# Kernel tuning notes

Hardware: AMD Instinct MI355X
Metric: run time of the kernel (lower is better)

Reference implementation:

```python
import jax, jax.numpy as jnp
import numpy as np

N_VERTICES = 2000
N_SENSORY = 784
N_EDGES = 500_000
BATCH = 32
T_STEPS = 5
LR_VALUES = 0.1


def setup_inputs() -> dict:
    key = jax.random.key(0)
    k1, k2, k3 = jax.random.split(key, 3)
    values = jax.random.normal(k1, (BATCH, N_VERTICES), dtype=jnp.float32)
    # weight_init 'normal 0.0' -> std = max(0.01, 0) = 0.01 in the torch module
    weights = jax.random.normal(k2, (N_EDGES,), dtype=jnp.float32) * 0.01
    edge_index = jax.random.randint(k3, (2, N_EDGES), 0, N_VERTICES, dtype=jnp.int32)
    # sensory nodes (first 784) are clamped; only internal nodes update
    update_mask = jnp.arange(N_VERTICES) >= N_SENSORY  # bool [N]
    return {
        "values": values,
        "weights": weights,
        "edge_index": edge_index,
        "update_mask": update_mask,
        "T": T_STEPS,
    }


def reference(values, weights, edge_index, update_mask, T):
    """Iterative predictive-coding message passing.

    Each step:
      pred_i  = sum_{e: dst(e)=i} w_e * f(values[src(e)])   (gather-mul-scatter)
      err     = values - pred
      back_j  = sum_{e: src(e)=j} w_e * err[dst(e)]          (reverse scatter)
      dv      = err - f'(values) * back                      (dE/dx)
      values  = values - lr * dv   (sensory nodes clamped)
    """
    src, dst = edge_index[0], edge_index[1]
    n = values.shape[1]
    mask = update_mask[None, :]

    def step(v, _):
        fx = jnp.tanh(v)                                   # [B, N]
        msg = weights[None, :] * fx[:, src]                # [B, E]
        pred = jax.ops.segment_sum(msg.T, dst, num_segments=n).T  # [B, N]
        err = v - pred                                     # [B, N]
        w_err = weights[None, :] * err[:, dst]             # [B, E]
        back = jax.ops.segment_sum(w_err.T, src, num_segments=n).T  # [B, N]
        fprime = 1.0 - fx * fx                             # tanh'
        dv = err - fprime * back
        v_new = jnp.where(mask, v - LR_VALUES * dv, v)
        return v_new, None

    v_final, _ = jax.lax.scan(step, values, None, length=T)
    return v_final
```

## Files before the change

### kernel.cpp

```cpp
#include <hip/hip_runtime.h>
#include <hip/hip_bf16.h>


#define N_V     2000
#define N_SENS  784
#define N_INT   (N_V - N_SENS)
#define N_E     500000
#define T_STEPS 5
#define LR_VAL  0.1f
#define NVB     (N_V * 32)
#define NVH     (N_V * 16)
#define KP      2016
#define NCH     63
#define NT1     125
#define NT2     76
#define FRAG_N  (2 * NCH * 64 * 8)
#define NBLK    250
#define EPB     2000
#define NBLK_P  NT1
#define BAR_STRIDE 32
#define BAR_N   ((NBLK_P + 1) * BAR_STRIDE)

typedef float  f32x4 __attribute__((ext_vector_type(4)));
typedef short  s16x8 __attribute__((ext_vector_type(8)));
typedef unsigned long long u64;

__device__ __forceinline__ float bits_to_f32(unsigned u) {
    union { unsigned u; float f; } c; c.u = u; return c.f;
}
__device__ __forceinline__ unsigned f32_to_bits(float f) {
    union { float f; unsigned u; } c; c.f = f; return c.u;
}
__device__ __forceinline__ unsigned short f32_to_bf16(float f) {
    unsigned u = f32_to_bits(f);
    return (unsigned short)((u + 0x7FFFu + ((u >> 16) & 1u)) >> 16);
}
__device__ __forceinline__ float bf16_to_f32(unsigned short s) {
    return bits_to_f32((unsigned)s << 16);
}

__device__ __forceinline__ u64 ald64(const void* p) {
    return __hip_atomic_load((const u64*)p, __ATOMIC_RELAXED,
                             __HIP_MEMORY_SCOPE_AGENT);
}
__device__ __forceinline__ void ast64(void* p, u64 v) {
    __hip_atomic_store((u64*)p, v, __ATOMIC_RELAXED, __HIP_MEMORY_SCOPE_AGENT);
}
__device__ __forceinline__ unsigned short ald16(const unsigned short* p) {
    return __hip_atomic_load(p, __ATOMIC_RELAXED, __HIP_MEMORY_SCOPE_AGENT);
}
__device__ __forceinline__ void ast16(unsigned short* p, unsigned short v) {
    __hip_atomic_store(p, v, __ATOMIC_RELAXED, __HIP_MEMORY_SCOPE_AGENT);
}
__device__ __forceinline__ int cohld(const int* p) {
    int v;
    asm volatile("global_load_dword %0, %1, off sc0 sc1\n\ts_waitcnt vmcnt(0)"
                 : "=v"(v) : "v"(p) : "memory");
    return v;
}
__device__ __forceinline__ void cohst(int* p, int v) {
    asm volatile("global_store_dword %0, %1, off sc0 sc1"
                 :: "v"(p), "v"(v) : "memory");
}

__device__ __forceinline__ int aposKB(int k, int b) {
    int c = k >> 5, q = (k >> 3) & 3, j = k & 7;
    int h = b >> 4, m = b & 15;
    return (((h * NCH + c) * 64) + q * 16 + m) * 8 + j;
}


__global__ __launch_bounds__(256) void k_cnt(const int* __restrict__ dst,
                                             int* __restrict__ cnt_g,
                                             unsigned short* __restrict__ fxA,
                                             unsigned short* __restrict__ errA,
                                             const float* __restrict__ vin,
                                             float* __restrict__ v,
                                             float* __restrict__ out,
                                             unsigned short* __restrict__ WAdT,
                                             int* __restrict__ bar) {
    __shared__ int cnt[NT1];
    int b = blockIdx.x;
    int t = b * 256 + threadIdx.x;
    {
        if (t < 16 * 32) {
            int k = 2000 + (t >> 5), bb = t & 31;
            fxA[aposKB(k, bb)] = 0;
            errA[aposKB(k, bb)] = 0;
        }
        if (t < N_INT * 2) {
            uint4 z = {0u, 0u, 0u, 0u};
            *(uint4*)(WAdT + (size_t)(t >> 1) * KP + 2000 + (t & 1) * 8) = z;
        }
        if (t < BAR_N) bar[t] = 0;
    }
    if (t < NVB) {
        float x = vin[t];
        int bb = t / N_V;
        int i = t - bb * N_V;
        v[(i << 5) + bb] = x;
        fxA[aposKB(i, bb)] = f32_to_bf16(tanhf(x));
        if (i < N_SENS) out[t] = x;
    }
    for (int i = threadIdx.x; i < NT1; i += 256) cnt[i] = 0;
    __syncthreads();
    int base = b * EPB;
    for (int e = base + threadIdx.x; e < base + EPB; e += 256)
        atomicAdd(&cnt[dst[e] >> 4], 1);
    __syncthreads();
    for (int tt = threadIdx.x; tt < NT1; tt += 256)
        cnt_g[tt * 256 + b] = cnt[tt];
}

__global__ __launch_bounds__(256) void k_scan_a(const int* __restrict__ cnt_g,
                                                int* __restrict__ base_g,
                                                int* __restrict__ totals) {
    __shared__ int sh[256];
    int t = blockIdx.x, tid = threadIdx.x;
    int v = (tid < NBLK) ? cnt_g[t * 256 + tid] : 0;
    sh[tid] = v;
    __syncthreads();
    for (int off = 1; off < 256; off <<= 1) {
        int x = (tid >= off) ? sh[tid - off] : 0;
        __syncthreads();
        sh[tid] += x;
        __syncthreads();
    }
    if (tid < NBLK) base_g[t * 256 + tid] = sh[tid] - v;
    if (tid == 255) totals[t] = sh[255];
}

__global__ __launch_bounds__(256) void k_place(
        const int* __restrict__ src, const int* __restrict__ dst,
        const float* __restrict__ w, const int* __restrict__ base_g,
        const int* __restrict__ totals, unsigned* __restrict__ pk_g) {
    __shared__ int cur[NT1];
    __shared__ int ts[NT1];
    int b = blockIdx.x;
    if (threadIdx.x == 0) {
        int a = 0;
        for (int t = 0; t < NT1; ++t) { ts[t] = a; a += totals[t]; }
    }
    __syncthreads();
    for (int t = threadIdx.x; t < NT1; t += 256)
        cur[t] = ts[t] + base_g[t * 256 + b];
    __syncthreads();
    int base = b * EPB;
    for (int e = base + threadIdx.x; e < base + EPB; e += 256) {
        int d = dst[e];
        unsigned pk = ((unsigned)f32_to_bf16(w[e]) << 16)
                    | ((unsigned)(d & 15) << 11) | (unsigned)src[e];
        int p = atomicAdd(&cur[d >> 4], 1);
        pk_g[p] = pk;
    }
}

__global__ __launch_bounds__(256) void k_build(
        const unsigned* __restrict__ pk_g, const int* __restrict__ totals,
        uint4* __restrict__ WAbf4, unsigned short* __restrict__ WAdT) {
    __shared__ float acc[16][KP];
    __shared__ int ts[NT1 + 1];
    int tile = blockIdx.x;
    for (int i = threadIdx.x; i < 16 * KP / 4; i += 256)
        ((float4*)&acc[0][0])[i] = make_float4(0.f, 0.f, 0.f, 0.f);
    if (threadIdx.x == 0) {
        int a = 0;
        for (int t = 0; t < NT1; ++t) { ts[t] = a; a += totals[t]; }
        ts[NT1] = a;
    }
    __syncthreads();
    int beg = ts[tile], end = ts[tile + 1];
    for (int e = beg + threadIdx.x; e < end; e += 256) {
        unsigned pk = pk_g[e];
        int row = (int)((pk >> 11) & 15u);
        atomicAdd(&acc[row][pk & 0x7FFu], bf16_to_f32((unsigned short)(pk >> 16)));
    }
    __syncthreads();
    for (int i = threadIdx.x; i < 16 * 252; i += 256) {
        int m = i / 252, g = i - m * 252;
        int c = g >> 2, q = g & 3;
        int col = g * 8;
        unsigned short r[8];
        #pragma unroll
        for (int j = 0; j < 8; ++j) r[j] = f32_to_bf16(acc[m][col + j]);
        WAbf4[((tile * NCH + c) * 64) + q * 16 + m] = *(const uint4*)r;
    }
    for (int i = threadIdx.x; i < N_INT; i += 256) {
        int j = N_SENS + i;
        unsigned short r[16];
        #pragma unroll
        for (int m = 0; m < 16; ++m) r[m] = f32_to_bf16(acc[m][j]);
        uint4* p = (uint4*)(WAdT + (size_t)i * KP + tile * 16);
        p[0] = *(const uint4*)r;
        p[1] = *(const uint4*)(r + 8);
    }
}

__device__ __forceinline__ void gbar(int* arr, int epoch, int bx, int tid) {
    asm volatile("s_waitcnt vmcnt(0) lgkmcnt(0)" ::: "memory");
    __syncthreads();
    if (bx == 0) {
        if (tid == 0) cohst(&arr[0], epoch);
        if (tid < NBLK_P) {
            while (cohld(&arr[tid * BAR_STRIDE]) < epoch)
                __builtin_amdgcn_s_sleep(2);
        }
        __syncthreads();
        if (tid == 0) cohst(&arr[NBLK_P * BAR_STRIDE], epoch);
    } else {
        if (tid == 0) {
            cohst(&arr[bx * BAR_STRIDE], epoch);
            while (cohld(&arr[NBLK_P * BAR_STRIDE]) < epoch)
                __builtin_amdgcn_s_sleep(2);
        }
        __syncthreads();
    }
}

__global__ __launch_bounds__(512, 1) void k_loop(
        const uint4* __restrict__ WAbf4, const unsigned short* __restrict__ WAdT,
        unsigned short* fxA, unsigned short* errA,
        float* v_cur, float* __restrict__ out, int* arr) {
    __shared__ uint4 WldsA[NCH * 64];
    __shared__ uint4 WldsB[NCH * 64];
    __shared__ float red[2600];
    const int bx = blockIdx.x, tid = threadIdx.x;
    {
        const uint4* Wg = WAbf4 + (size_t)bx * (NCH * 64);
        for (int i = tid; i < NCH * 64; i += 512) WldsA[i] = Wg[i];
        if (bx < NT2) {
            for (int i = tid; i < NCH * 64; i += 512) {
                int c = i >> 6, ll = i & 63;
                int row = bx * 16 + (ll & 15);
                int k0 = c * 32 + (ll >> 4) * 8;
                WldsB[i] = *(const uint4*)(WAdT + (size_t)row * KP + k0);
            }
        }
    }
    const int w = tid >> 6, l = tid & 63;
    const int h = w >> 2, w4 = w & 3;
    const int cbeg = w4 * 16;
    float* my = &red[h * 1300 + w4 * 325 + l * 5];
    int epoch = 0;
    __syncthreads();

    for (int t = 0; t < T_STEPS; ++t) {
        {
            const u64* ap = (const u64*)fxA
                          + ((size_t)h * (NCH * 64) + cbeg * 64 + l) * 2;
            u64 f0[16], f1[16];
            #pragma unroll
            for (int cc = 0; cc < 16; ++cc)
                if (cbeg + cc < NCH) {
                    f0[cc] = ald64(ap + cc * 128);
                    f1[cc] = ald64(ap + cc * 128 + 1);
                }
            __builtin_amdgcn_sched_barrier(0);
            f32x4 acc = {0.f, 0.f, 0.f, 0.f};
            #pragma unroll
            for (int cc = 0; cc < 16; ++cc)
                if (cbeg + cc < NCH) {
                    u64 d[2] = {f0[cc], f1[cc]};
                    uint4 bfrag = WldsA[(cbeg + cc) * 64 + l];
                    acc = __builtin_amdgcn_mfma_f32_16x16x32_bf16(
                              *(s16x8*)d, *(s16x8*)&bfrag, acc, 0, 0, 0);
                }
            #pragma unroll
            for (int r = 0; r < 4; ++r) my[r] = acc[r];
            __syncthreads();
            if (w4 == 0) {
                float s[4];
                #pragma unroll
                for (int r = 0; r < 4; ++r)
                    s[r] = red[h * 1300 + l * 5 + r] + red[h * 1300 + 325 + l * 5 + r]
                         + red[h * 1300 + 650 + l * 5 + r] + red[h * 1300 + 975 + l * 5 + r];
                int i = bx * 16 + (l & 15);
                int q = l >> 4;
                int c2 = i >> 5, q2 = (i >> 3) & 3, j2 = i & 7;
                const float* vp = v_cur + (i << 5) + h * 16 + q * 4;
                union { u64 u[2]; float f[4]; } vu;
                vu.u[0] = ald64(vp);
                vu.u[1] = ald64(vp + 2);
                int base = ((h * NCH + c2) * 64 + q2 * 16) * 8 + j2;
                #pragma unroll
                for (int r = 0; r < 4; ++r)
                    ast16(&errA[base + (q * 4 + r) * 8],
                          f32_to_bf16(vu.f[r] - s[r]));
            }
        }
        ++epoch; gbar(arr, epoch, bx, tid);

        if (bx < NT2) {
            const u64* ap = (const u64*)errA
                          + ((size_t)h * (NCH * 64) + cbeg * 64 + l) * 2;
            u64 f0[16], f1[16];
            #pragma unroll
            for (int cc = 0; cc < 16; ++cc)
                if (cbeg + cc < NCH) {
                    f0[cc] = ald64(ap + cc * 128);
                    f1[cc] = ald64(ap + cc * 128 + 1);
                }
            __builtin_amdgcn_sched_barrier(0);
            f32x4 acc = {0.f, 0.f, 0.f, 0.f};
            #pragma unroll
            for (int cc = 0; cc < 16; ++cc)
                if (cbeg + cc < NCH) {
                    u64 d[2] = {f0[cc], f1[cc]};
                    uint4 bfrag = WldsB[(cbeg + cc) * 64 + l];
                    acc = __builtin_amdgcn_mfma_f32_16x16x32_bf16(
                              *(s16x8*)d, *(s16x8*)&bfrag, acc, 0, 0, 0);
                }
            #pragma unroll
            for (int r = 0; r < 4; ++r) my[r] = acc[r];
            __syncthreads();
            if (w4 == 0) {
                float s[4];
                #pragma unroll
                for (int r = 0; r < 4; ++r)
                    s[r] = red[h * 1300 + l * 5 + r] + red[h * 1300 + 325 + l * 5 + r]
                         + red[h * 1300 + 650 + l * 5 + r] + red[h * 1300 + 975 + l * 5 + r];
                int j = N_SENS + bx * 16 + (l & 15);
                int q = l >> 4;
                int c2 = j >> 5, q2 = (j >> 3) & 3, j2 = j & 7;
                float* vp = v_cur + (j << 5) + h * 16 + q * 4;
                union { u64 u[2]; float f[4]; } vu;
                vu.u[0] = ald64(vp);
                vu.u[1] = ald64(vp + 2);
                int base = ((h * NCH + c2) * 64 + q2 * 16) * 8 + j2;
                #pragma unroll
                for (int r = 0; r < 4; ++r) {
                    float e0 = bf16_to_f32(ald16(&errA[base + (q * 4 + r) * 8]));
                    float fxv = tanhf(vu.f[r]);
                    float vn = vu.f[r] - LR_VAL * (e0 - (1.f - fxv * fxv) * s[r]);
                    vu.f[r] = vn;
                    ast16(&fxA[base + (q * 4 + r) * 8], f32_to_bf16(tanhf(vn)));
                }
                ast64(vp, vu.u[0]);
                ast64(vp + 2, vu.u[1]);
                if (t == T_STEPS - 1) {
                    #pragma unroll
                    for (int r = 0; r < 4; ++r) {
                        int b = h * 16 + q * 4 + r;
                        out[b * N_V + j] = vu.f[r];
                    }
                }
            }
        }
        if (t < T_STEPS - 1) { ++epoch; gbar(arr, epoch, bx, tid); }
    }
}


__global__ void k_zero_i32(int* a, int n) {
    int t = blockIdx.x * blockDim.x + threadIdx.x;
    if (t < n) a[t] = 0;
}

__global__ void k_hist(const int* __restrict__ src, const int* __restrict__ dst,
                       int* cnt_dst, int* cnt_src) {
    int e = blockIdx.x * blockDim.x + threadIdx.x;
    if (e < N_E) {
        atomicAdd(&cnt_dst[dst[e]], 1);
        atomicAdd(&cnt_src[src[e]], 1);
    }
}

__global__ __launch_bounds__(1024) void k_scan(int* cnt_a, int* rp_a,
                                               int* cnt_b, int* rp_b) {
    __shared__ int sh[1024];
    int t = threadIdx.x;
    for (int pass = 0; pass < 2; ++pass) {
        int* cnt = pass ? cnt_b : cnt_a;
        int* rp  = pass ? rp_b  : rp_a;
        int i0 = 2 * t, i1 = 2 * t + 1;
        int c0 = (i0 < N_V) ? cnt[i0] : 0;
        int c1 = (i1 < N_V) ? cnt[i1] : 0;
        __syncthreads();
        sh[t] = c0 + c1;
        __syncthreads();
        for (int off = 1; off < 1024; off <<= 1) {
            int v = (t >= off) ? sh[t - off] : 0;
            __syncthreads();
            sh[t] += v;
            __syncthreads();
        }
        int incl = sh[t];
        int e0 = incl - (c0 + c1);
        int e1 = e0 + c0;
        if (i0 <= N_V) rp[i0] = e0;
        if (i1 <= N_V) rp[i1] = e1;
        if (i0 < N_V) cnt[i0] = e0;
        if (i1 < N_V) cnt[i1] = e1;
    }
}

__global__ void k_scatter(const int* __restrict__ src, const int* __restrict__ dst,
                          const float* __restrict__ w,
                          int* cur_dst, int* cur_src,
                          unsigned* __restrict__ pk_dst, unsigned* __restrict__ pk_src) {
    int e = blockIdx.x * blockDim.x + threadIdx.x;
    if (e < N_E) {
        int s = src[e], d = dst[e];
        unsigned wbits = (unsigned)f32_to_bf16(w[e]);
        int p = atomicAdd(&cur_dst[d], 1);
        pk_dst[p] = (wbits << 16) | (unsigned)s;
        int q = atomicAdd(&cur_src[s], 1);
        pk_src[q] = (wbits << 16) | (unsigned)d;
    }
}

__global__ void k_cast_in(const float* __restrict__ vin, float* __restrict__ v) {
    int t = blockIdx.x * blockDim.x + threadIdx.x;
    if (t < NVB) {
        int i = t >> 5, b = t & 31;
        v[t] = vin[b * N_V + i];
    }
}

__global__ void k_fx_csr(const float* __restrict__ v, unsigned short* __restrict__ fx) {
    int t = blockIdx.x * blockDim.x + threadIdx.x;
    if (t < NVB) {
        int i = t >> 5, b = t & 31;
        int h = b >> 4, b16 = b & 15;
        fx[h * NVH + i * 16 + b16] = f32_to_bf16(tanhf(v[t]));
    }
}

__global__ __launch_bounds__(256) void k_pred_err(
        const float* __restrict__ v, const unsigned short* __restrict__ fx,
        const int* __restrict__ rp, const unsigned* __restrict__ pk,
        unsigned short* __restrict__ err) {
    __shared__ unsigned short tab[NVH];
    int h  = blockIdx.x / 250;
    int vg = blockIdx.x % 250;
    {
        const uint4* g = (const uint4*)(fx + h * NVH);
        uint4* l = (uint4*)tab;
        for (int i = threadIdx.x; i < NVH / 8; i += 256) l[i] = g[i];
    }
    __syncthreads();
    int wave = threadIdx.x >> 6;
    int lane = threadIdx.x & 63;
    int b16 = lane & 15, epar = lane >> 4;
    for (int k = 0; k < 2; ++k) {
        int vid = vg * 8 + wave * 2 + k;
        int beg = rp[vid], end = rp[vid + 1];
        float sum = 0.f;
        for (int e = beg + epar; e < end; e += 4) {
            unsigned p = pk[e];
            float w = bits_to_f32(p & 0xFFFF0000u);
            int nb = (int)(p & 0xFFFFu);
            sum += w * bf16_to_f32(tab[nb * 16 + b16]);
        }
        sum += __shfl_xor(sum, 16, 64);
        sum += __shfl_xor(sum, 32, 64);
        if (epar == 0) {
            float vo = v[(vid << 5) + h * 16 + b16];
            err[h * NVH + vid * 16 + b16] = f32_to_bf16(vo - sum);
        }
    }
}

__global__ __launch_bounds__(256) void k_back_upd(
        const unsigned short* __restrict__ fx, const unsigned short* __restrict__ err,
        const int* __restrict__ rp, const unsigned* __restrict__ pk,
        float* __restrict__ v) {
    __shared__ unsigned short tab[NVH];
    int h  = blockIdx.x / 152;
    int vg = blockIdx.x % 152;
    {
        const uint4* g = (const uint4*)(err + h * NVH);
        uint4* l = (uint4*)tab;
        for (int i = threadIdx.x; i < NVH / 8; i += 256) l[i] = g[i];
    }
    __syncthreads();
    int wave = threadIdx.x >> 6;
    int lane = threadIdx.x & 63;
    int b16 = lane & 15, epar = lane >> 4;
    for (int k = 0; k < 2; ++k) {
        int vid = N_SENS + vg * 8 + wave * 2 + k;
        if (vid >= N_V) continue;
        int beg = rp[vid], end = rp[vid + 1];
        float sum = 0.f;
        for (int e = beg + epar; e < end; e += 4) {
            unsigned p = pk[e];
            float w = bits_to_f32(p & 0xFFFF0000u);
            int nb = (int)(p & 0xFFFFu);
            sum += w * bf16_to_f32(tab[nb * 16 + b16]);
        }
        sum += __shfl_xor(sum, 16, 64);
        sum += __shfl_xor(sum, 32, 64);
        if (epar == 0) {
            float e0  = bf16_to_f32(tab[vid * 16 + b16]);
            float fxv = bf16_to_f32(fx[h * NVH + vid * 16 + b16]);
            float dv = e0 - (1.f - fxv * fxv) * sum;
            v[(vid << 5) + h * 16 + b16] -= LR_VAL * dv;
        }
    }
}

__global__ void k_out_fb(const float* __restrict__ v, float* __restrict__ out) {
    int t = blockIdx.x * blockDim.x + threadIdx.x;
    if (t < NVB) {
        int b = t / N_V;
        int i = t - b * N_V;
        out[t] = v[(i << 5) + b];
    }
}


extern "C" void kernel_launch(void* const* d_in, const int* in_sizes, int n_in,
                              void* d_out, int out_size, void* d_ws, size_t ws_size,
                              hipStream_t stream) {
    const float* vals = (const float*)d_in[0];
    const float* wts  = (const float*)d_in[1];
    const int* ei = (const int*)d_in[2];
    const int* src = ei;
    const int* dst = ei + N_E;
    float* out = (float*)d_out;

    const int EB = (N_E + 255) / 256;

    const size_t WABF_T = (size_t)NT1 * NCH * 64;
    const size_t WADT_N = (size_t)N_INT * KP;
    const size_t need = (size_t)N_E * 4 + 2 * NT1 * 256 * 4 + 512
                      + WADT_N * 2 + WABF_T * 16
                      + 2 * (size_t)FRAG_N * 2 + NVB * 4
                      + (size_t)BAR_N * 4 + 256;

    if (ws_size >= need) {
        unsigned* pk_g = (unsigned*)d_ws;
        int* cnt_g  = (int*)(pk_g + N_E);
        int* base_g = cnt_g + NT1 * 256;
        int* totals = base_g + NT1 * 256;
        unsigned short* WAdT = (unsigned short*)(totals + 128);
        uint4* WAbf4 = (uint4*)(WAdT + WADT_N);
        unsigned short* fxA  = (unsigned short*)(WAbf4 + WABF_T);
        unsigned short* errA = fxA + FRAG_N;
        float* v_cur = (float*)(errA + FRAG_N);
        int* bar_arr = (int*)(v_cur + NVB);

        k_cnt<<<NBLK, 256, 0, stream>>>(dst, cnt_g, fxA, errA, vals, v_cur,
                                        out, WAdT, bar_arr);
        k_scan_a<<<NT1, 256, 0, stream>>>(cnt_g, base_g, totals);
        k_place<<<NBLK, 256, 0, stream>>>(src, dst, wts, base_g, totals, pk_g);
        k_build<<<NT1, 256, 0, stream>>>(pk_g, totals, WAbf4, WAdT);
        k_loop<<<NBLK_P, 512, 0, stream>>>(WAbf4, WAdT, fxA, errA, v_cur, out,
                                           bar_arr);
    } else {
        float* v_cur = (float*)d_ws;
        unsigned short* fx_g  = (unsigned short*)(v_cur + NVB);
        unsigned short* err_g = fx_g + NVB;
        int* rp_dst  = (int*)(err_g + NVB);
        int* rp_src  = rp_dst + 2048;
        int* cur_dst = rp_src + 2048;
        int* cur_src = cur_dst + 2048;
        unsigned* pk_dst = (unsigned*)(cur_src + 2048);
        unsigned* pk_src = pk_dst + N_E;

        k_zero_i32<<<16, 256, 0, stream>>>(cur_dst, 4096);
        k_hist<<<EB, 256, 0, stream>>>(src, dst, cur_dst, cur_src);
        k_scan<<<1, 1024, 0, stream>>>(cur_dst, rp_dst, cur_src, rp_src);
        k_scatter<<<EB, 256, 0, stream>>>(src, dst, wts, cur_dst, cur_src,
                                          pk_dst, pk_src);
        k_cast_in<<<250, 256, 0, stream>>>(vals, v_cur);
        for (int t = 0; t < T_STEPS; ++t) {
            k_fx_csr<<<250, 256, 0, stream>>>(v_cur, fx_g);
            k_pred_err<<<500, 256, 0, stream>>>(v_cur, fx_g, rp_dst, pk_dst, err_g);
            k_back_upd<<<304, 256, 0, stream>>>(fx_g, err_g, rp_src, pk_src, v_cur);
        }
        k_out_fb<<<250, 256, 0, stream>>>(v_cur, out);
    }
}
```

Measured before the change: 153.6 us.

## Fuse preprocessing kernels into persistent loop kernel with grid barriers

Merges the count, scan, place and build preprocessing kernels into the persistent iteration kernel. The phases are separated by software grid barriers, and the weight-build LDS buffer is unioned with the per-block weight tiles. This removes four kernel launches and their inter-kernel gaps, at the cost of grid-barrier synchronisation and atomic (coherent) global accesses for data passed between phases. The preprocessing now runs on 125 blocks of 512 threads instead of 250 blocks of 256.

```diff
diff --git a/kernel.cpp b/kernel.cpp
--- a/kernel.cpp
+++ b/kernel.cpp
@@ -15,8 +15,7 @@
 #define NT1     125
 #define NT2     76
 #define FRAG_N  (2 * NCH * 64 * 8)
-#define NBLK    250
-#define EPB     2000
+#define EPB2    4000
 #define NBLK_P  NT1
 #define BAR_STRIDE 32
 #define BAR_N   ((NBLK_P + 1) * BAR_STRIDE)
@@ -50,6 +49,15 @@
     return __hip_atomic_load(p, __ATOMIC_RELAXED, __HIP_MEMORY_SCOPE_AGENT);
 }
 __device__ __forceinline__ void ast16(unsigned short* p, unsigned short v) {
+    __hip_atomic_store(p, v, __ATOMIC_RELAXED, __HIP_MEMORY_SCOPE_AGENT);
+}
+__device__ __forceinline__ int ali32(const int* p) {
+    return __hip_atomic_load(p, __ATOMIC_RELAXED, __HIP_MEMORY_SCOPE_AGENT);
+}
+__device__ __forceinline__ void asi32(int* p, int v) {
+    __hip_atomic_store(p, v, __ATOMIC_RELAXED, __HIP_MEMORY_SCOPE_AGENT);
+}
+__device__ __forceinline__ void ast32(float* p, float v) {
     __hip_atomic_store(p, v, __ATOMIC_RELAXED, __HIP_MEMORY_SCOPE_AGENT);
 }
 __device__ __forceinline__ int cohld(const int* p) {
@@ -67,133 +75,6 @@
     int c = k >> 5, q = (k >> 3) & 3, j = k & 7;
     int h = b >> 4, m = b & 15;
     return (((h * NCH + c) * 64) + q * 16 + m) * 8 + j;
-}
-
-
-__global__ __launch_bounds__(256) void k_cnt(const int* __restrict__ dst,
-                                             int* __restrict__ cnt_g,
-                                             unsigned short* __restrict__ fxA,
-                                             unsigned short* __restrict__ errA,
-                                             const float* __restrict__ vin,
-                                             float* __restrict__ v,
-                                             float* __restrict__ out,
-                                             unsigned short* __restrict__ WAdT,
-                                             int* __restrict__ bar) {
-    __shared__ int cnt[NT1];
-    int b = blockIdx.x;
-    int t = b * 256 + threadIdx.x;
-    {
-        if (t < 16 * 32) {
-            int k = 2000 + (t >> 5), bb = t & 31;
-            fxA[aposKB(k, bb)] = 0;
-            errA[aposKB(k, bb)] = 0;
-        }
-        if (t < N_INT * 2) {
-            uint4 z = {0u, 0u, 0u, 0u};
-            *(uint4*)(WAdT + (size_t)(t >> 1) * KP + 2000 + (t & 1) * 8) = z;
-        }
-        if (t < BAR_N) bar[t] = 0;
-    }
-    if (t < NVB) {
-        float x = vin[t];
-        int bb = t / N_V;
-        int i = t - bb * N_V;
-        v[(i << 5) + bb] = x;
-        fxA[aposKB(i, bb)] = f32_to_bf16(tanhf(x));
-        if (i < N_SENS) out[t] = x;
-    }
-    for (int i = threadIdx.x; i < NT1; i += 256) cnt[i] = 0;
-    __syncthreads();
-    int base = b * EPB;
-    for (int e = base + threadIdx.x; e < base + EPB; e += 256)
-        atomicAdd(&cnt[dst[e] >> 4], 1);
-    __syncthreads();
-    for (int tt = threadIdx.x; tt < NT1; tt += 256)
-        cnt_g[tt * 256 + b] = cnt[tt];
-}
-
-__global__ __launch_bounds__(256) void k_scan_a(const int* __restrict__ cnt_g,
-                                                int* __restrict__ base_g,
-                                                int* __restrict__ totals) {
-    __shared__ int sh[256];
-    int t = blockIdx.x, tid = threadIdx.x;
-    int v = (tid < NBLK) ? cnt_g[t * 256 + tid] : 0;
-    sh[tid] = v;
-    __syncthreads();
-    for (int off = 1; off < 256; off <<= 1) {
-        int x = (tid >= off) ? sh[tid - off] : 0;
-        __syncthreads();
-        sh[tid] += x;
-        __syncthreads();
-    }
-    if (tid < NBLK) base_g[t * 256 + tid] = sh[tid] - v;
-    if (tid == 255) totals[t] = sh[255];
-}
-
-__global__ __launch_bounds__(256) void k_place(
-        const int* __restrict__ src, const int* __restrict__ dst,
-        const float* __restrict__ w, const int* __restrict__ base_g,
-        const int* __restrict__ totals, unsigned* __restrict__ pk_g) {
-    __shared__ int cur[NT1];
-    __shared__ int ts[NT1];
-    int b = blockIdx.x;
-    if (threadIdx.x == 0) {
-        int a = 0;
-        for (int t = 0; t < NT1; ++t) { ts[t] = a; a += totals[t]; }
-    }
-    __syncthreads();
-    for (int t = threadIdx.x; t < NT1; t += 256)
-        cur[t] = ts[t] + base_g[t * 256 + b];
-    __syncthreads();
-    int base = b * EPB;
-    for (int e = base + threadIdx.x; e < base + EPB; e += 256) {
-        int d = dst[e];
-        unsigned pk = ((unsigned)f32_to_bf16(w[e]) << 16)
-                    | ((unsigned)(d & 15) << 11) | (unsigned)src[e];
-        int p = atomicAdd(&cur[d >> 4], 1);
-        pk_g[p] = pk;
-    }
-}
-
-__global__ __launch_bounds__(256) void k_build(
-        const unsigned* __restrict__ pk_g, const int* __restrict__ totals,
-        uint4* __restrict__ WAbf4, unsigned short* __restrict__ WAdT) {
-    __shared__ float acc[16][KP];
-    __shared__ int ts[NT1 + 1];
-    int tile = blockIdx.x;
-    for (int i = threadIdx.x; i < 16 * KP / 4; i += 256)
-        ((float4*)&acc[0][0])[i] = make_float4(0.f, 0.f, 0.f, 0.f);
-    if (threadIdx.x == 0) {
-        int a = 0;
-        for (int t = 0; t < NT1; ++t) { ts[t] = a; a += totals[t]; }
-        ts[NT1] = a;
-    }
-    __syncthreads();
-    int beg = ts[tile], end = ts[tile + 1];
-    for (int e = beg + threadIdx.x; e < end; e += 256) {
-        unsigned pk = pk_g[e];
-        int row = (int)((pk >> 11) & 15u);
-        atomicAdd(&acc[row][pk & 0x7FFu], bf16_to_f32((unsigned short)(pk >> 16)));
-    }
-    __syncthreads();
-    for (int i = threadIdx.x; i < 16 * 252; i += 256) {
-        int m = i / 252, g = i - m * 252;
-        int c = g >> 2, q = g & 3;
-        int col = g * 8;
-        unsigned short r[8];
-        #pragma unroll
-        for (int j = 0; j < 8; ++j) r[j] = f32_to_bf16(acc[m][col + j]);
-        WAbf4[((tile * NCH + c) * 64) + q * 16 + m] = *(const uint4*)r;
-    }
-    for (int i = threadIdx.x; i < N_INT; i += 256) {
-        int j = N_SENS + i;
-        unsigned short r[16];
-        #pragma unroll
-        for (int m = 0; m < 16; ++m) r[m] = f32_to_bf16(acc[m][j]);
-        uint4* p = (uint4*)(WAdT + (size_t)i * KP + tile * 16);
-        p[0] = *(const uint4*)r;
-        p[1] = *(const uint4*)(r + 8);
-    }
 }
 
 __device__ __forceinline__ void gbar(int* arr, int epoch, int bx, int tid) {
@@ -217,23 +98,147 @@
     }
 }
 
-__global__ __launch_bounds__(512, 1) void k_loop(
-        const uint4* __restrict__ WAbf4, const unsigned short* __restrict__ WAdT,
+__global__ void k_zero_i32(int* a, int n) {
+    int t = blockIdx.x * blockDim.x + threadIdx.x;
+    if (t < n) a[t] = 0;
+}
+
+__global__ __launch_bounds__(512, 1) void k_all(
+        const int* __restrict__ src, const int* __restrict__ dst,
+        const float* __restrict__ wts, const float* __restrict__ vin,
+        int* cnt_g, int* base_g, int* totals, unsigned* pk_g,
+        uint4* WAbf4, unsigned short* WAdT,
         unsigned short* fxA, unsigned short* errA,
-        float* v_cur, float* __restrict__ out, int* arr) {
-    __shared__ uint4 WldsA[NCH * 64];
-    __shared__ uint4 WldsB[NCH * 64];
+        float* v_cur, float* out, int* arr) {
+    union LdsU {
+        float acc[16][KP];
+        struct { uint4 A[NCH * 64]; uint4 B[NCH * 64]; } w;
+    };
+    __shared__ LdsU U;
     __shared__ float red[2600];
+    __shared__ int sh_scan[128];
+    __shared__ int ts[NT1 + 1];
+    __shared__ int cur[NT1];
+    __shared__ int cnt_l[NT1];
+
     const int bx = blockIdx.x, tid = threadIdx.x;
+    int epoch = 0;
+
+    {
+        int t = bx * 512 + tid;
+        if (t < 16 * 32) {
+            int k = 2000 + (t >> 5), bb = t & 31;
+            ast16(&fxA[aposKB(k, bb)], 0);
+            ast16(&errA[aposKB(k, bb)], 0);
+        }
+        if (t < N_INT * 2) {
+            u64* p = (u64*)(WAdT + (size_t)(t >> 1) * KP + 2000 + (t & 1) * 8);
+            ast64(p, 0); ast64(p + 1, 0);
+        }
+        {
+            float x = vin[t];
+            int bb = t / N_V;
+            int i = t - bb * N_V;
+            ast32(&v_cur[(i << 5) + bb], x);
+            ast16(&fxA[aposKB(i, bb)], f32_to_bf16(tanhf(x)));
+            if (i < N_SENS) ast32(&out[t], x);
+        }
+        if (tid < NT1) cnt_l[tid] = 0;
+        __syncthreads();
+        int base = bx * EPB2;
+        for (int e = base + tid; e < base + EPB2; e += 512)
+            atomicAdd(&cnt_l[dst[e] >> 4], 1);
+        __syncthreads();
+        if (tid < NT1) asi32(&cnt_g[tid * 128 + bx], cnt_l[tid]);
+    }
+    ++epoch; gbar(arr, epoch, bx, tid);
+
+    {
+        int v = 0;
+        if (tid < NT1) v = ali32(&cnt_g[bx * 128 + tid]);
+        if (tid < 128) sh_scan[tid] = v;
+        __syncthreads();
+        for (int off = 1; off < 128; off <<= 1) {
+            int x = (tid >= off && tid < 128) ? sh_scan[tid - off] : 0;
+            __syncthreads();
+            if (tid < 128) sh_scan[tid] += x;
+            __syncthreads();
+        }
+        if (tid < NT1) asi32(&base_g[bx * 128 + tid], sh_scan[tid] - v);
+        if (tid == NT1 - 1) asi32(&totals[bx], sh_scan[NT1 - 1]);
+    }
+    ++epoch; gbar(arr, epoch, bx, tid);
+
+    {
+        int v = 0;
+        if (tid < NT1) v = ali32(&totals[tid]);
+        if (tid < 128) sh_scan[tid] = v;
+        __syncthreads();
+        for (int off = 1; off < 128; off <<= 1) {
+            int x = (tid >= off && tid < 128) ? sh_scan[tid - off] : 0;
+            __syncthreads();
+            if (tid < 128) sh_scan[tid] += x;
+            __syncthreads();
+        }
+        if (tid < NT1) ts[tid] = sh_scan[tid] - v;
+        if (tid == NT1 - 1) ts[NT1] = sh_scan[NT1 - 1];
+        __syncthreads();
+        if (tid < NT1) cur[tid] = ts[tid] + ali32(&base_g[tid * 128 + bx]);
+        __syncthreads();
+        int base = bx * EPB2;
+        for (int e = base + tid; e < base + EPB2; e += 512) {
+            int d = dst[e];
+            unsigned pk = ((unsigned)f32_to_bf16(wts[e]) << 16)
+                        | ((unsigned)(d & 15) << 11) | (unsigned)src[e];
+            int p = atomicAdd(&cur[d >> 4], 1);
+            asi32((int*)&pk_g[p], (int)pk);
+        }
+    }
+    ++epoch; gbar(arr, epoch, bx, tid);
+
+    {
+        for (int i = tid; i < 16 * KP / 4; i += 512)
+            ((float4*)&U.acc[0][0])[i] = make_float4(0.f, 0.f, 0.f, 0.f);
+        __syncthreads();
+        int beg = ts[bx], end = ts[bx + 1];
+        for (int e = beg + tid; e < end; e += 512) {
+            unsigned pk = (unsigned)ali32((const int*)&pk_g[e]);
+            atomicAdd(&U.acc[(pk >> 11) & 15][pk & 0x7FFu],
+                      bf16_to_f32((unsigned short)(pk >> 16)));
+        }
+        __syncthreads();
+        for (int i = tid; i < 16 * 252; i += 512) {
+            int m = i / 252, g = i - m * 252;
+            int c = g >> 2, q = g & 3;
+            int col = g * 8;
+            unsigned short r[8];
+            #pragma unroll
+            for (int j = 0; j < 8; ++j) r[j] = f32_to_bf16(U.acc[m][col + j]);
+            WAbf4[((bx * NCH + c) * 64) + q * 16 + m] = *(const uint4*)r;
+        }
+        for (int i = tid; i < N_INT; i += 512) {
+            union { unsigned short s[16]; u64 u[4]; } cc;
+            #pragma unroll
+            for (int m = 0; m < 16; ++m) cc.s[m] = f32_to_bf16(U.acc[m][N_SENS + i]);
+            u64* p = (u64*)(WAdT + (size_t)i * KP + bx * 16);
+            ast64(p, cc.u[0]); ast64(p + 1, cc.u[1]);
+            ast64(p + 2, cc.u[2]); ast64(p + 3, cc.u[3]);
+        }
+    }
+    ++epoch; gbar(arr, epoch, bx, tid);
+
     {
         const uint4* Wg = WAbf4 + (size_t)bx * (NCH * 64);
-        for (int i = tid; i < NCH * 64; i += 512) WldsA[i] = Wg[i];
+        for (int i = tid; i < NCH * 64; i += 512) U.w.A[i] = Wg[i];
         if (bx < NT2) {
             for (int i = tid; i < NCH * 64; i += 512) {
                 int c = i >> 6, ll = i & 63;
                 int row = bx * 16 + (ll & 15);
                 int k0 = c * 32 + (ll >> 4) * 8;
-                WldsB[i] = *(const uint4*)(WAdT + (size_t)row * KP + k0);
+                const u64* p = (const u64*)(WAdT + (size_t)row * KP + k0);
+                union { u64 u[2]; uint4 q; } cc;
+                cc.u[0] = ald64(p); cc.u[1] = ald64(p + 1);
+                U.w.B[i] = cc.q;
             }
         }
     }
@@ -241,7 +246,6 @@
     const int h = w >> 2, w4 = w & 3;
     const int cbeg = w4 * 16;
     float* my = &red[h * 1300 + w4 * 325 + l * 5];
-    int epoch = 0;
     __syncthreads();
 
     for (int t = 0; t < T_STEPS; ++t) {
@@ -261,7 +265,7 @@
             for (int cc = 0; cc < 16; ++cc)
                 if (cbeg + cc < NCH) {
                     u64 d[2] = {f0[cc], f1[cc]};
-                    uint4 bfrag = WldsA[(cbeg + cc) * 64 + l];
+                    uint4 bfrag = U.w.A[(cbeg + cc) * 64 + l];
                     acc = __builtin_amdgcn_mfma_f32_16x16x32_bf16(
                               *(s16x8*)d, *(s16x8*)&bfrag, acc, 0, 0, 0);
                 }
@@ -306,7 +310,7 @@
             for (int cc = 0; cc < 16; ++cc)
                 if (cbeg + cc < NCH) {
                     u64 d[2] = {f0[cc], f1[cc]};
-                    uint4 bfrag = WldsB[(cbeg + cc) * 64 + l];
+                    uint4 bfrag = U.w.B[(cbeg + cc) * 64 + l];
                     acc = __builtin_amdgcn_mfma_f32_16x16x32_bf16(
                               *(s16x8*)d, *(s16x8*)&bfrag, acc, 0, 0, 0);
                 }
@@ -341,7 +345,7 @@
                     #pragma unroll
                     for (int r = 0; r < 4; ++r) {
                         int b = h * 16 + q * 4 + r;
-                        out[b * N_V + j] = vu.f[r];
+                        ast32(&out[b * N_V + j], vu.f[r]);
                     }
                 }
             }
@@ -350,11 +354,6 @@
     }
 }
 
-
-__global__ void k_zero_i32(int* a, int n) {
-    int t = blockIdx.x * blockDim.x + threadIdx.x;
-    if (t < n) a[t] = 0;
-}
 
 __global__ void k_hist(const int* __restrict__ src, const int* __restrict__ dst,
                        int* cnt_dst, int* cnt_src) {
@@ -523,7 +522,7 @@
 
     const size_t WABF_T = (size_t)NT1 * NCH * 64;
     const size_t WADT_N = (size_t)N_INT * KP;
-    const size_t need = (size_t)N_E * 4 + 2 * NT1 * 256 * 4 + 512
+    const size_t need = (size_t)N_E * 4 + 2 * NT1 * 128 * 4 + 512
                       + WADT_N * 2 + WABF_T * 16
                       + 2 * (size_t)FRAG_N * 2 + NVB * 4
                       + (size_t)BAR_N * 4 + 256;
@@ -531,8 +530,8 @@
     if (ws_size >= need) {
         unsigned* pk_g = (unsigned*)d_ws;
         int* cnt_g  = (int*)(pk_g + N_E);
-        int* base_g = cnt_g + NT1 * 256;
-        int* totals = base_g + NT1 * 256;
+        int* base_g = cnt_g + NT1 * 128;
+        int* totals = base_g + NT1 * 128;
         unsigned short* WAdT = (unsigned short*)(totals + 128);
         uint4* WAbf4 = (uint4*)(WAdT + WADT_N);
         unsigned short* fxA  = (unsigned short*)(WAbf4 + WABF_T);
@@ -540,13 +539,11 @@
         float* v_cur = (float*)(errA + FRAG_N);
         int* bar_arr = (int*)(v_cur + NVB);
 
-        k_cnt<<<NBLK, 256, 0, stream>>>(dst, cnt_g, fxA, errA, vals, v_cur,
-                                        out, WAdT, bar_arr);
-        k_scan_a<<<NT1, 256, 0, stream>>>(cnt_g, base_g, totals);
-        k_place<<<NBLK, 256, 0, stream>>>(src, dst, wts, base_g, totals, pk_g);
-        k_build<<<NT1, 256, 0, stream>>>(pk_g, totals, WAbf4, WAdT);
-        k_loop<<<NBLK_P, 512, 0, stream>>>(WAbf4, WAdT, fxA, errA, v_cur, out,
-                                           bar_arr);
+        k_zero_i32<<<16, 256, 0, stream>>>(bar_arr, BAR_N);
+        k_all<<<NBLK_P, 512, 0, stream>>>(src, dst, wts, vals,
+                                          cnt_g, base_g, totals, pk_g,
+                                          WAbf4, WAdT, fxA, errA,
+                                          v_cur, out, bar_arr);
     } else {
         float* v_cur = (float*)d_ws;
         unsigned short* fx_g  = (unsigned short*)(v_cur + NVB);
```

Result: slower. 169.8 us (+10.6%).

## Split each tile's two batch halves across separate blocks, doubling the grid

Applied to the files above, without the earlier changes.

The persistent loop kernel now launches two blocks per 16-row tile, one per batch half (h = bx & 1), instead of one block handling both halves with four waves each. Each block's eight waves split the K chunks eight ways, so every wave issues fewer MFMAs and the LDS reduction sums eight partials. This doubles the number of blocks taking part in the software grid barrier to 250, which spreads work over more CUs but adds barrier participants and duplicates the weight-tile loads into LDS.

```diff
diff --git a/kernel.cpp b/kernel.cpp
--- a/kernel.cpp
+++ b/kernel.cpp
@@ -17,7 +17,7 @@
 #define FRAG_N  (2 * NCH * 64 * 8)
 #define NBLK    250
 #define EPB     2000
-#define NBLK_P  NT1
+#define NBLK_P  250
 #define BAR_STRIDE 32
 #define BAR_N   ((NBLK_P + 1) * BAR_STRIDE)
 
@@ -225,22 +225,22 @@
     __shared__ uint4 WldsB[NCH * 64];
     __shared__ float red[2600];
     const int bx = blockIdx.x, tid = threadIdx.x;
+    const int tile = bx >> 1, h = bx & 1;
     {
-        const uint4* Wg = WAbf4 + (size_t)bx * (NCH * 64);
+        const uint4* Wg = WAbf4 + (size_t)tile * (NCH * 64);
         for (int i = tid; i < NCH * 64; i += 512) WldsA[i] = Wg[i];
-        if (bx < NT2) {
+        if (bx < 2 * NT2) {
             for (int i = tid; i < NCH * 64; i += 512) {
                 int c = i >> 6, ll = i & 63;
-                int row = bx * 16 + (ll & 15);
+                int row = tile * 16 + (ll & 15);
                 int k0 = c * 32 + (ll >> 4) * 8;
                 WldsB[i] = *(const uint4*)(WAdT + (size_t)row * KP + k0);
             }
         }
     }
     const int w = tid >> 6, l = tid & 63;
-    const int h = w >> 2, w4 = w & 3;
-    const int cbeg = w4 * 16;
-    float* my = &red[h * 1300 + w4 * 325 + l * 5];
+    const int cbeg = w * 8;
+    float* my = &red[w * 325 + l * 5];
     int epoch = 0;
     __syncthreads();
 
@@ -248,9 +248,9 @@
         {
             const u64* ap = (const u64*)fxA
                           + ((size_t)h * (NCH * 64) + cbeg * 64 + l) * 2;
-            u64 f0[16], f1[16];
+            u64 f0[8], f1[8];
             #pragma unroll
-            for (int cc = 0; cc < 16; ++cc)
+            for (int cc = 0; cc < 8; ++cc)
                 if (cbeg + cc < NCH) {
                     f0[cc] = ald64(ap + cc * 128);
                     f1[cc] = ald64(ap + cc * 128 + 1);
@@ -258,7 +258,7 @@
             __builtin_amdgcn_sched_barrier(0);
             f32x4 acc = {0.f, 0.f, 0.f, 0.f};
             #pragma unroll
-            for (int cc = 0; cc < 16; ++cc)
+            for (int cc = 0; cc < 8; ++cc)
                 if (cbeg + cc < NCH) {
                     u64 d[2] = {f0[cc], f1[cc]};
                     uint4 bfrag = WldsA[(cbeg + cc) * 64 + l];
@@ -268,13 +268,17 @@
             #pragma unroll
             for (int r = 0; r < 4; ++r) my[r] = acc[r];
             __syncthreads();
-            if (w4 == 0) {
+            if (w == 0) {
                 float s[4];
                 #pragma unroll
-                for (int r = 0; r < 4; ++r)
-                    s[r] = red[h * 1300 + l * 5 + r] + red[h * 1300 + 325 + l * 5 + r]
-                         + red[h * 1300 + 650 + l * 5 + r] + red[h * 1300 + 975 + l * 5 + r];
-                int i = bx * 16 + (l & 15);
+                for (int r = 0; r < 4; ++r) {
+                    float sum = 0.f;
+                    #pragma unroll
+                    for (int ww = 0; ww < 8; ++ww)
+                        sum += red[ww * 325 + l * 5 + r];
+                    s[r] = sum;
+                }
+                int i = tile * 16 + (l & 15);
                 int q = l >> 4;
                 int c2 = i >> 5, q2 = (i >> 3) & 3, j2 = i & 7;
                 const float* vp = v_cur + (i << 5) + h * 16 + q * 4;
@@ -290,12 +294,12 @@
         }
         ++epoch; gbar(arr, epoch, bx, tid);
 
-        if (bx < NT2) {
+        if (bx < 2 * NT2) {
             const u64* ap = (const u64*)errA
                           + ((size_t)h * (NCH * 64) + cbeg * 64 + l) * 2;
-            u64 f0[16], f1[16];
+            u64 f0[8], f1[8];
             #pragma unroll
-            for (int cc = 0; cc < 16; ++cc)
+            for (int cc = 0; cc < 8; ++cc)
                 if (cbeg + cc < NCH) {
                     f0[cc] = ald64(ap + cc * 128);
                     f1[cc] = ald64(ap + cc * 128 + 1);
@@ -303,7 +307,7 @@
             __builtin_amdgcn_sched_barrier(0);
             f32x4 acc = {0.f, 0.f, 0.f, 0.f};
             #pragma unroll
-            for (int cc = 0; cc < 16; ++cc)
+            for (int cc = 0; cc < 8; ++cc)
                 if (cbeg + cc < NCH) {
                     u64 d[2] = {f0[cc], f1[cc]};
                     uint4 bfrag = WldsB[(cbeg + cc) * 64 + l];
@@ -313,13 +317,17 @@
             #pragma unroll
             for (int r = 0; r < 4; ++r) my[r] = acc[r];
             __syncthreads();
-            if (w4 == 0) {
+            if (w == 0) {
                 float s[4];
                 #pragma unroll
-                for (int r = 0; r < 4; ++r)
-                    s[r] = red[h * 1300 + l * 5 + r] + red[h * 1300 + 325 + l * 5 + r]
-                         + red[h * 1300 + 650 + l * 5 + r] + red[h * 1300 + 975 + l * 5 + r];
-                int j = N_SENS + bx * 16 + (l & 15);
+                for (int r = 0; r < 4; ++r) {
+                    float sum = 0.f;
+                    #pragma unroll
+                    for (int ww = 0; ww < 8; ++ww)
+                        sum += red[ww * 325 + l * 5 + r];
+                    s[r] = sum;
+                }
+                int j = N_SENS + tile * 16 + (l & 15);
                 int q = l >> 4;
                 int c2 = j >> 5, q2 = (j >> 3) & 3, j2 = j & 7;
                 float* vp = v_cur + (j << 5) + h * 16 + q * 4;
```

New measurement: 149.5 us. -2.6%, faster.
